# Optimization experiments

Measured on AMD Instinct MI355X. Metric: run time of the kernel, lower is better.

Reference implementation:

```python
import jax, jax.numpy as jnp
import numpy as np

HID, H, KV, D = 2048, 16, 4, 128
B, L = 8, 1024
T = B * L
EPS = 1e-6
NEG = -1e9


def _rms(x, w):
    # RMSNorm over head_dim in fp32
    var = jnp.mean(x.astype(jnp.float32) ** 2, axis=-1, keepdims=True)
    return (x.astype(jnp.float32) * jax.lax.rsqrt(var + EPS)).astype(x.dtype) * w


def _rot_half(x):
    x1, x2 = jnp.split(x, 2, axis=-1)
    return jnp.concatenate([-x2, x1], axis=-1)


def setup_inputs() -> dict:
    key = jax.random.key(0)
    ks = jax.random.split(key, 24)
    inp = {}
    inp['packed_sequence'] = jax.random.normal(ks[0], (T, HID), jnp.float32) * 0.02
    # RoPE tables: positions restart per sample
    pos = jnp.tile(jnp.arange(L, dtype=jnp.float32), B)  # [T]
    inv_freq = 1.0 / (10000.0 ** (jnp.arange(0, D, 2, dtype=jnp.float32) / D))
    ang = pos[:, None] * inv_freq[None, :]  # [T, D/2]
    inp['cos'] = jnp.concatenate([jnp.cos(ang), jnp.cos(ang)], axis=-1)
    inp['sin'] = jnp.concatenate([jnp.sin(ang), jnp.sin(ang)], axis=-1)
    # per-sample causal additive mask [B, L, L]
    causal = jnp.tril(jnp.ones((L, L), bool))
    inp['attn_bias'] = jnp.broadcast_to(jnp.where(causal, 0.0, NEG).astype(jnp.float32), (B, L, L))
    inp['gen_mask'] = jax.random.randint(ks[1], (T,), 0, 2, jnp.int32)
    s = 0.02
    inp['Wq'] = jax.random.normal(ks[2], (H * D, HID), jnp.float32) * s
    inp['bq'] = jnp.zeros((H * D,), jnp.float32)
    inp['Wqg'] = jax.random.normal(ks[3], (H * D, HID), jnp.float32) * s
    inp['bqg'] = jnp.zeros((H * D,), jnp.float32)
    inp['Wk'] = jax.random.normal(ks[4], (KV * D, HID), jnp.float32) * s
    inp['bk'] = jnp.zeros((KV * D,), jnp.float32)
    inp['Wkg'] = jax.random.normal(ks[5], (KV * D, HID), jnp.float32) * s
    inp['bkg'] = jnp.zeros((KV * D,), jnp.float32)
    inp['Wv'] = jax.random.normal(ks[6], (KV * D, HID), jnp.float32) * s
    inp['bv'] = jnp.zeros((KV * D,), jnp.float32)
    inp['Wvg'] = jax.random.normal(ks[7], (KV * D, HID), jnp.float32) * s
    inp['bvg'] = jnp.zeros((KV * D,), jnp.float32)
    inp['Wo'] = jax.random.normal(ks[8], (HID, H * D), jnp.float32) * s
    inp['Wog'] = jax.random.normal(ks[9], (HID, H * D), jnp.float32) * s
    inp['q_norm_w'] = jnp.ones((D,), jnp.float32)
    inp['q_norm_gen_w'] = jnp.ones((D,), jnp.float32)
    inp['k_norm_w'] = jnp.ones((D,), jnp.float32)
    inp['k_norm_gen_w'] = jnp.ones((D,), jnp.float32)
    return inp


def reference(packed_sequence, cos, sin, attn_bias, gen_mask,
              Wq, bq, Wqg, bqg, Wk, bk, Wkg, bkg, Wv, bv, Wvg, bvg,
              Wo, Wog, q_norm_w, q_norm_gen_w, k_norm_w, k_norm_gen_w):
    route = (gen_mask > 0)[:, None]  # [T,1]; und/gen indexes partition tokens -> select
    # dual-path QKV projections (scatter into zero buffers == per-token select)
    q = jnp.where(route, packed_sequence @ Wqg.T + bqg, packed_sequence @ Wq.T + bq)
    k = jnp.where(route, packed_sequence @ Wkg.T + bkg, packed_sequence @ Wk.T + bk)
    v = jnp.where(route, packed_sequence @ Wvg.T + bvg, packed_sequence @ Wv.T + bv)
    q = q.reshape(T, H, D)
    k = k.reshape(T, KV, D)
    v = v.reshape(T, KV, D)
    rh = route[:, :, None]  # [T,1,1]
    # dual-path per-head-dim RMSNorm
    q = jnp.where(rh, _rms(q, q_norm_gen_w), _rms(q, q_norm_w))
    k = jnp.where(rh, _rms(k, k_norm_gen_w), _rms(k, k_norm_w))
    # RoPE (broadcast over heads, unsqueeze_dim=1)
    c, s = cos[:, None, :], sin[:, None, :]
    q = q * c + _rot_half(q) * s
    k = k * c + _rot_half(k) * s
    # GQA: repeat kv heads to H
    k = jnp.repeat(k, H // KV, axis=1)
    v = jnp.repeat(v, H // KV, axis=1)
    # ragged attention, equal sample lens -> batched SDPA with per-sample masks
    qb = q.reshape(B, L, H, D)
    kb = k.reshape(B, L, H, D)
    vb = v.reshape(B, L, H, D)
    scores = jnp.einsum('blhd,bmhd->bhlm', qb, kb) / np.sqrt(D).astype(np.float32)
    scores = scores + attn_bias[:, None, :, :]
    p = jax.nn.softmax(scores, axis=-1)
    o = jnp.einsum('bhlm,bmhd->blhd', p, vb).reshape(T, H * D)
    # dual-path output projection (no bias)
    return jnp.where(route, o @ Wog.T, o @ Wo.T)
```

## Files before the change

kernel.cpp:

```cpp
#include <hip/hip_runtime.h>

#define T_TOK 8192
#define HID   2048
#define NH    16
#define NKV   4
#define HD    128

typedef __attribute__((ext_vector_type(8))) short short8;
typedef __attribute__((ext_vector_type(4))) float f32x4;
typedef __attribute__((ext_vector_type(4))) unsigned short us4;

__device__ __forceinline__ unsigned short f2b(float f) {
  union { float f; unsigned int u; } x; x.f = f;
  unsigned int u = x.u;
  return (unsigned short)((u + 0x7FFFu + ((u >> 16) & 1u)) >> 16);
}
__device__ __forceinline__ float b2f(unsigned short u) {
  union { float f; unsigned int u; } x; x.u = ((unsigned int)u) << 16; return x.f;
}

__device__ __forceinline__ void ld_lds16(const unsigned short* g, unsigned short* l) {
  __builtin_amdgcn_global_load_lds(
      (const __attribute__((address_space(1))) unsigned int*)g,
      (__attribute__((address_space(3))) unsigned int*)l, 16, 0, 0);
}

__global__ __launch_bounds__(1024) void scan_route(const int* __restrict__ gm,
                                                   int* __restrict__ perm,
                                                   int* __restrict__ n0p) {
  __shared__ int cnt[1024];
  int tid = threadIdx.x;
  int base = tid * 8;
  int r[8]; int c0 = 0;
#pragma unroll
  for (int i = 0; i < 8; i++) { r[i] = gm[base + i] > 0 ? 1 : 0; c0 += 1 - r[i]; }
  cnt[tid] = c0;
  __syncthreads();
  for (int off = 1; off < 1024; off <<= 1) {
    int add = (tid >= off) ? cnt[tid - off] : 0;
    __syncthreads();
    cnt[tid] += add;
    __syncthreads();
  }
  int incl = cnt[tid];
  int total0 = cnt[1023];
  int p0 = incl - c0;
  int p1 = total0 + (base - (incl - c0));
#pragma unroll
  for (int i = 0; i < 8; i++) {
    int t = base + i;
    if (r[i] == 0) perm[p0++] = t;
    else           perm[p1++] = t;
  }
  if (tid == 0) n0p[0] = total0;
}

struct ConvArgs {
  const float* src[9];
  unsigned short* dst[9];
  int blk_end[9];
};

__global__ __launch_bounds__(256) void convert_all(ConvArgs a) {
  int blk = blockIdx.x;
  int s = 0;
  while (blk >= a.blk_end[s]) s++;
  int local = blk - (s ? a.blk_end[s - 1] : 0);
  int i = local * 1024 + threadIdx.x * 4;
  float4 v = *(const float4*)(a.src[s] + i);
  us4 o = { f2b(v.x), f2b(v.y), f2b(v.z), f2b(v.w) };
  *(us4*)(a.dst[s] + i) = o;
}

#define BM  128
#define BK  64

__device__ __forceinline__ void gemm_core(
    const unsigned short* __restrict__ Xb,
    const unsigned short* __restrict__ W,
    const float* __restrict__ bias,
    const int* __restrict__ perm,
    int r0, int r1, int col0, int N,
    float* __restrict__ outF, unsigned short* __restrict__ outB,
    unsigned short* As, unsigned short* Bs)
{
  int tid = threadIdx.x;
  int lane = tid & 63, wid = tid >> 6;
  int quad = lane >> 4, l15 = lane & 15;
  int wr = (wid >> 1) * 64, wc = (wid & 1) * 64;
  int lrow = lane >> 3;
  int sc8 = (lane & 7) ^ (lrow & 7);

  const unsigned short* ag[4]; const unsigned short* bg[4];
  unsigned short* al[4]; unsigned short* bl[4];
#pragma unroll
  for (int i = 0; i < 4; i++) {
    int row = wid * 32 + i * 8 + lrow;
    int gr = r0 + row; if (gr > r1 - 1) gr = r1 - 1;
    ag[i] = Xb + (size_t)perm[gr] * HID + sc8 * 8;
    bg[i] = W + (size_t)(col0 + row) * HID + sc8 * 8;
    al[i] = As + (wid * 32 + i * 8) * BK;
    bl[i] = Bs + (wid * 32 + i * 8) * BK;
  }

  f32x4 zero = {0.f, 0.f, 0.f, 0.f};
  f32x4 acc[4][4];
#pragma unroll
  for (int a = 0; a < 4; a++)
#pragma unroll
    for (int b = 0; b < 4; b++) acc[a][b] = zero;

  for (int k0 = 0; k0 < HID; k0 += BK) {
#pragma unroll
    for (int i = 0; i < 4; i++) {
      ld_lds16(ag[i] + k0, al[i]);
      ld_lds16(bg[i] + k0, bl[i]);
    }
    __syncthreads();
#pragma unroll
    for (int kk = 0; kk < 2; kk++) {
      int cswz = ((kk * 4 + quad) ^ (l15 & 7)) * 8;
      short8 af[4], bf[4];
#pragma unroll
      for (int mt = 0; mt < 4; mt++)
        af[mt] = *(const short8*)&As[(wr + mt * 16 + l15) * BK + cswz];
#pragma unroll
      for (int nt = 0; nt < 4; nt++)
        bf[nt] = *(const short8*)&Bs[(wc + nt * 16 + l15) * BK + cswz];
#pragma unroll
      for (int mt = 0; mt < 4; mt++)
#pragma unroll
        for (int nt = 0; nt < 4; nt++)
          acc[mt][nt] = __builtin_amdgcn_mfma_f32_16x16x32_bf16(af[mt], bf[nt], acc[mt][nt], 0, 0, 0);
    }
    __syncthreads();
  }

#pragma unroll
  for (int mt = 0; mt < 4; mt++) {
#pragma unroll
    for (int r = 0; r < 4; r++) {
      int lr = wr + mt * 16 + quad * 4 + r;
      int gr = r0 + lr;
      if (gr >= r1) continue;
      int tok = perm[gr];
#pragma unroll
      for (int nt = 0; nt < 4; nt++) {
        int col = col0 + wc + nt * 16 + l15;
        float v = acc[mt][nt][r];
        if (bias) v += bias[col];
        if (outF) outF[(size_t)tok * N + col] = v;
        else      outB[(size_t)tok * N + col] = f2b(v);
      }
    }
  }
}

__global__ __launch_bounds__(256, 3) void gemm_qkv(
    const unsigned short* __restrict__ xb,
    const unsigned short* wq0, const unsigned short* wq1,
    const float* bq0, const float* bq1,
    const unsigned short* wk0, const unsigned short* wk1,
    const float* bk0, const float* bk1,
    const unsigned short* wv0, const unsigned short* wv1,
    const float* bv0, const float* bv1,
    unsigned short* qraw, unsigned short* kraw, unsigned short* vb,
    const int* __restrict__ perm, const int* __restrict__ n0p)
{
  __shared__ unsigned short As[BM * BK];
  __shared__ unsigned short Bs[BM * BK];
  int set = blockIdx.z;
  int n0 = n0p[0];
  int r0, r1;
  if (set == 0) { r0 = blockIdx.x * BM; if (r0 >= n0) return; r1 = (r0 + BM < n0) ? r0 + BM : n0; }
  else          { r0 = n0 + blockIdx.x * BM; if (r0 >= T_TOK) return; r1 = (r0 + BM < T_TOK) ? r0 + BM : T_TOK; }
  int y = blockIdx.y;
  const unsigned short* w; const float* bias;
  unsigned short* ob; int col0, N;
  if (y < 16)      { w = set ? wq1 : wq0; bias = set ? bq1 : bq0; col0 = y * 128;        N = HID; ob = qraw; }
  else if (y < 20) { w = set ? wk1 : wk0; bias = set ? bk1 : bk0; col0 = (y - 16) * 128; N = 512; ob = kraw; }
  else             { w = set ? wv1 : wv0; bias = set ? bv1 : bv0; col0 = (y - 20) * 128; N = 512; ob = vb; }
  gemm_core(xb, w, bias, perm, r0, r1, col0, N, nullptr, ob, As, Bs);
}

__global__ __launch_bounds__(256, 3) void gemm_out(
    const unsigned short* __restrict__ obuf,
    const unsigned short* wo0, const unsigned short* wo1,
    float* __restrict__ out,
    const int* __restrict__ perm, const int* __restrict__ n0p)
{
  __shared__ unsigned short As[BM * BK];
  __shared__ unsigned short Bs[BM * BK];
  int set = blockIdx.z;
  int n0 = n0p[0];
  int r0, r1;
  if (set == 0) { r0 = blockIdx.x * BM; if (r0 >= n0) return; r1 = (r0 + BM < n0) ? r0 + BM : n0; }
  else          { r0 = n0 + blockIdx.x * BM; if (r0 >= T_TOK) return; r1 = (r0 + BM < T_TOK) ? r0 + BM : T_TOK; }
  gemm_core(obuf, set ? wo1 : wo0, nullptr, perm, r0, r1, blockIdx.y * 128, HID, out, nullptr, As, Bs);
}

__global__ __launch_bounds__(256) void rms_rope_all(
    const unsigned short* __restrict__ qin, unsigned short* __restrict__ qout,
    const unsigned short* __restrict__ kin, unsigned short* __restrict__ kout,
    const float* __restrict__ cosb, const float* __restrict__ sinb,
    const int* __restrict__ gm,
    const float* __restrict__ qwn, const float* __restrict__ qwg,
    const float* __restrict__ kwn, const float* __restrict__ kwg)
{
  int wvid = blockIdx.x * 4 + (threadIdx.x >> 6);
  int lane = threadIdx.x & 63;
  const unsigned short* in; unsigned short* outp;
  const float* wn; const float* wg; int t, h, nh;
  if (wvid < T_TOK * NH) {
    in = qin; outp = qout; wn = qwn; wg = qwg; t = wvid >> 4; h = wvid & 15; nh = NH;
  } else {
    int w2 = wvid - T_TOK * NH;
    in = kin; outp = kout; wn = kwn; wg = kwg; t = w2 >> 2; h = w2 & 3; nh = NKV;
  }
  size_t off = ((size_t)t * nh + h) * HD;
  float x1 = b2f(in[off + lane]), x2 = b2f(in[off + 64 + lane]);
  float ss = x1 * x1 + x2 * x2;
#pragma unroll
  for (int o = 32; o > 0; o >>= 1) ss += __shfl_xor(ss, o, 64);
  float inv = rsqrtf(ss * (1.0f / 128.0f) + 1e-6f);
  const float* w = (gm[t] > 0) ? wg : wn;
  float n1 = x1 * inv * w[lane];
  float n2 = x2 * inv * w[lane + 64];
  float c1 = cosb[t * HD + lane],      s1 = sinb[t * HD + lane];
  float c2 = cosb[t * HD + 64 + lane], s2 = sinb[t * HD + 64 + lane];
  outp[off + lane]      = f2b(n1 * c1 - n2 * s1);
  outp[off + 64 + lane] = f2b(n2 * c2 + n1 * s2);
}

__global__ __launch_bounds__(256) void vtrans(const unsigned short* __restrict__ vb,
                                              unsigned short* __restrict__ vt) {
  __shared__ unsigned short Vs[64][136];
  int kt = blockIdx.x, kvh = blockIdx.y, b = blockIdx.z;
  int t = threadIdx.x;
  int kv0 = kt * 64;
  int key = t >> 2, c0 = t & 3;
#pragma unroll
  for (int i = 0; i < 4; i++) {
    int cc = c0 * 4 + i;
    *(short8*)&Vs[key][cc * 8] =
        *(const short8*)(vb + ((size_t)(b * 1024 + kv0 + key) * NKV + kvh) * HD + cc * 8);
  }
  __syncthreads();
  int d = t >> 1, hh = t & 1;
  unsigned short tmp[32];
#pragma unroll
  for (int k = 0; k < 32; k++) tmp[k] = Vs[hh * 32 + k][d];
  size_t base = ((size_t)(b * NKV + kvh) * HD + d) * 1024 + kv0 + hh * 32;
  *(short8*)(vt + base)      = *(short8*)&tmp[0];
  *(short8*)(vt + base + 8)  = *(short8*)&tmp[8];
  *(short8*)(vt + base + 16) = *(short8*)&tmp[16];
  *(short8*)(vt + base + 24) = *(short8*)&tmp[24];
}

__global__ __launch_bounds__(512, 4) void attn_kernel(
    const unsigned short* __restrict__ qb,
    const unsigned short* __restrict__ kb,
    const unsigned short* __restrict__ vt,
    unsigned short* __restrict__ ob)
{
  __shared__ unsigned short Ks[2][64 * 128];
  __shared__ unsigned short Vt[2][128 * 64];
  __shared__ unsigned short Ps[8 * 16 * 64];
  int pslot = blockIdx.x, kvh = blockIdx.y, b = blockIdx.z;
  int tid = threadIdx.x, lane = tid & 63, wid = tid >> 6;
  int quad = lane >> 4, l15 = lane & 15;
  int h = kvh * 4 + (wid >> 1);
  int g = wid & 1;
  const float sc = 0.088388347648318447f;
  f32x4 zero = {0.f, 0.f, 0.f, 0.f};

  int skey = (wid << 2) + (lane >> 4);
  int kswz = ((lane & 15) ^ (skey & 7)) * 8;
  int sd   = (wid << 3) + (lane >> 3);
  int vswz = ((lane & 7) ^ (sd & 7)) * 8;

  auto stageKV = [&](int buf, int kv0) {
#pragma unroll
    for (int i = 0; i < 2; i++) {
      int key = i * 32 + skey;
      ld_lds16(kb + ((size_t)(b * 1024 + kv0 + key) * NKV + kvh) * HD + kswz,
               &Ks[buf][(size_t)(i * 32 + (wid << 2)) * 128]);
    }
#pragma unroll
    for (int i = 0; i < 2; i++) {
      int d = i * 64 + sd;
      ld_lds16(vt + ((size_t)(b * NKV + kvh) * HD + d) * 1024 + kv0 + vswz,
               &Vt[buf][(size_t)(i * 64 + (wid << 3)) * 64]);
    }
  };

  for (int half = 0; half < 2; half++) {
    int a = half ? (31 - pslot) : pslot;
    int q0 = a * 32;
    int qrow = q0 + g * 16 + l15;
    size_t qoff = ((size_t)(b * 1024 + qrow) * NH + h) * HD;
    short8 qfr[4];
#pragma unroll
    for (int kk = 0; kk < 4; kk++)
      qfr[kk] = *(const short8*)(qb + qoff + kk * 32 + quad * 8);

    f32x4 oacc[8];
#pragma unroll
    for (int i = 0; i < 8; i++) oacc[i] = zero;
    float lpart[4] = {0.f, 0.f, 0.f, 0.f};

    int ktiles = a / 2 + 1;
    stageKV(0, 0);
    int cur = 0;

    for (int kt = 0; kt < ktiles; kt++) {
      int kv0 = kt * 64;
      bool hasnext = (kt + 1 < ktiles);
      if (hasnext) {
        stageKV(cur ^ 1, kv0 + 64);
        asm volatile("s_waitcnt vmcnt(4)" ::: "memory");
      } else {
        asm volatile("s_waitcnt vmcnt(0)" ::: "memory");
      }
      __builtin_amdgcn_s_barrier();
      __builtin_amdgcn_sched_barrier(0);
      const unsigned short* ksb = Ks[cur];
      const unsigned short* vvb = Vt[cur];
      bool lastt = (kt == ktiles - 1);

      f32x4 s[4];
      __builtin_amdgcn_s_setprio(1);
#pragma unroll
      for (int g4 = 0; g4 < 4; g4++) {
        f32x4 acc = zero;
#pragma unroll
        for (int kk = 0; kk < 4; kk++) {
          short8 bfr = *(const short8*)&ksb[(g4 * 16 + l15) * 128 + ((kk * 4 + quad) ^ (l15 & 7)) * 8];
          acc = __builtin_amdgcn_mfma_f32_16x16x32_bf16(qfr[kk], bfr, acc, 0, 0, 0);
        }
        s[g4] = acc;
      }
      __builtin_amdgcn_s_setprio(0);

      int rowb = q0 + g * 16 + quad * 4;
#pragma unroll
      for (int g4 = 0; g4 < 4; g4++) {
        int col = kv0 + g4 * 16 + l15;
        int k8 = g4 * 2 + (l15 >> 3);
#pragma unroll
        for (int r = 0; r < 4; r++) {
          float p = __expf(s[g4][r] * sc);
          if (lastt && col > rowb + r) p = 0.f;
          lpart[r] += p;
          int row = quad * 4 + r;
          Ps[wid * 1024 + row * 64 + ((k8 ^ (row & 7)) * 8 + (l15 & 7))] = f2b(p);
        }
      }

      __builtin_amdgcn_s_setprio(1);
#pragma unroll
      for (int kk = 0; kk < 2; kk++) {
        short8 pa = *(const short8*)&Ps[wid * 1024 + l15 * 64 + ((kk * 4 + quad) ^ (l15 & 7)) * 8];
#pragma unroll
        for (int dg = 0; dg < 8; dg++) {
          short8 vf = *(const short8*)&vvb[(dg * 16 + l15) * 64 + ((kk * 4 + quad) ^ (l15 & 7)) * 8];
          oacc[dg] = __builtin_amdgcn_mfma_f32_16x16x32_bf16(pa, vf, oacc[dg], 0, 0, 0);
        }
      }
      __builtin_amdgcn_s_setprio(0);

      __builtin_amdgcn_s_barrier();
      __builtin_amdgcn_sched_barrier(0);
      cur ^= 1;
    }

#pragma unroll
    for (int r = 0; r < 4; r++) {
      float v = lpart[r];
#pragma unroll
      for (int o = 8; o > 0; o >>= 1) v += __shfl_xor(v, o, 64);
      lpart[r] = 1.0f / v;
    }
#pragma unroll
    for (int dg = 0; dg < 8; dg++)
#pragma unroll
      for (int r = 0; r < 4; r++) {
        int row = q0 + g * 16 + quad * 4 + r;
        ob[((size_t)(b * 1024 + row) * NH + h) * HD + dg * 16 + l15] =
            f2b(oacc[dg][r] * lpart[r]);
      }
  }
}

extern "C" void kernel_launch(void* const* d_in, const int* in_sizes, int n_in,
                              void* d_out, int out_size, void* d_ws, size_t ws_size,
                              hipStream_t stream) {
  const float* x    = (const float*)d_in[0];
  const float* cosb = (const float*)d_in[1];
  const float* sinb = (const float*)d_in[2];
  const int*   gm   = (const int*)d_in[4];
  const float* Wq   = (const float*)d_in[5];
  const float* bq   = (const float*)d_in[6];
  const float* Wqg  = (const float*)d_in[7];
  const float* bqg  = (const float*)d_in[8];
  const float* Wk   = (const float*)d_in[9];
  const float* bk   = (const float*)d_in[10];
  const float* Wkg  = (const float*)d_in[11];
  const float* bkg  = (const float*)d_in[12];
  const float* Wv   = (const float*)d_in[13];
  const float* bv   = (const float*)d_in[14];
  const float* Wvg  = (const float*)d_in[15];
  const float* bvg  = (const float*)d_in[16];
  const float* Wo   = (const float*)d_in[17];
  const float* Wog  = (const float*)d_in[18];
  const float* qnw  = (const float*)d_in[19];
  const float* qngw = (const float*)d_in[20];
  const float* knw  = (const float*)d_in[21];
  const float* kngw = (const float*)d_in[22];
  float* out = (float*)d_out;

  char* wsb = (char*)d_ws;
  size_t off = 0;
  auto alloc = [&](size_t bytes) -> char* {
    char* p = wsb + off;
    off += (bytes + 255) & ~(size_t)255;
    return p;
  };
  int* perm = (int*)alloc((size_t)T_TOK * 4);
  int* n0p  = (int*)alloc(4);
  unsigned short* xb  = (unsigned short*)alloc((size_t)T_TOK * HID * 2);
  unsigned short* wq0 = (unsigned short*)alloc((size_t)HID * HID * 2);
  unsigned short* wq1 = (unsigned short*)alloc((size_t)HID * HID * 2);
  unsigned short* wk0 = (unsigned short*)alloc((size_t)512 * HID * 2);
  unsigned short* wk1 = (unsigned short*)alloc((size_t)512 * HID * 2);
  unsigned short* wv0 = (unsigned short*)alloc((size_t)512 * HID * 2);
  unsigned short* wv1 = (unsigned short*)alloc((size_t)512 * HID * 2);
  unsigned short* wo0 = (unsigned short*)alloc((size_t)HID * HID * 2);
  unsigned short* wo1 = (unsigned short*)alloc((size_t)HID * HID * 2);
  unsigned short* qraw = (unsigned short*)alloc((size_t)T_TOK * HID * 2);
  unsigned short* kraw = (unsigned short*)alloc((size_t)T_TOK * 512 * 2);
  unsigned short* vbuf = (unsigned short*)alloc((size_t)T_TOK * 512 * 2);
  unsigned short* vtb  = (unsigned short*)alloc((size_t)T_TOK * 512 * 2);
  unsigned short* qbuf = (unsigned short*)alloc((size_t)T_TOK * HID * 2);
  unsigned short* kbuf = (unsigned short*)alloc((size_t)T_TOK * 512 * 2);
  unsigned short* obuf = qraw;

  scan_route<<<dim3(1), dim3(1024), 0, stream>>>(gm, perm, n0p);

  ConvArgs ca;
  const float* srcs[9] = {x, Wq, Wqg, Wk, Wkg, Wv, Wvg, Wo, Wog};
  unsigned short* dsts[9] = {xb, wq0, wq1, wk0, wk1, wv0, wv1, wo0, wo1};
  int ns[9] = {T_TOK * HID, HID * HID, HID * HID, 512 * HID, 512 * HID,
               512 * HID, 512 * HID, HID * HID, HID * HID};
  int cum = 0;
  for (int i = 0; i < 9; i++) {
    ca.src[i] = srcs[i]; ca.dst[i] = dsts[i];
    cum += ns[i] / 1024; ca.blk_end[i] = cum;
  }
  convert_all<<<dim3(cum), dim3(256), 0, stream>>>(ca);

  gemm_qkv<<<dim3(64, 24, 2), dim3(256), 0, stream>>>(
      xb, wq0, wq1, bq, bqg, wk0, wk1, bk, bkg, wv0, wv1, bv, bvg,
      qraw, kraw, vbuf, perm, n0p);

  rms_rope_all<<<dim3(T_TOK * (NH + NKV) / 4), dim3(256), 0, stream>>>(
      qraw, qbuf, kraw, kbuf, cosb, sinb, gm, qnw, qngw, knw, kngw);
  vtrans<<<dim3(16, 4, 8), dim3(256), 0, stream>>>(vbuf, vtb);

  attn_kernel<<<dim3(16, 4, 8), dim3(512), 0, stream>>>(qbuf, kbuf, vtb, obuf);

  gemm_out<<<dim3(64, 16, 2), dim3(256), 0, stream>>>(obuf, wo0, wo1, out, perm, n0p);
}
```

Measured before the change: 567.2 us.

## Rewrite projection GEMMs as 256x256 double-buffered 8-wave pipelined kernel

Replaces the 128x128 single-buffered GEMM core with a 256x256 tile computed by 8 waves, using double-buffered LDS and staggered async global->LDS loads interleaved with MFMA phases, plus s_setprio around the math. The goal is to hide global load latency behind compute and raise data reuse per tile, cutting the per-iteration barrier stalls of the old kernel. It uses 128KB of LDS per block and larger accumulators, which lowers occupancy. Bigger tiles also waste more work on the partial tiles at the route-split boundary.

```diff
diff --git a/kernel.cpp b/kernel.cpp
--- a/kernel.cpp
+++ b/kernel.cpp
@@ -72,10 +72,11 @@
   *(us4*)(a.dst[s] + i) = o;
 }
 
-#define BM  128
-#define BK  64
-
-__device__ __forceinline__ void gemm_core(
+#define BM2 256
+#define BK2 64
+#define NT2 (HID / BK2)
+
+__device__ __forceinline__ void gemm8(
     const unsigned short* __restrict__ Xb,
     const unsigned short* __restrict__ W,
     const float* __restrict__ bias,
@@ -87,67 +88,108 @@
   int tid = threadIdx.x;
   int lane = tid & 63, wid = tid >> 6;
   int quad = lane >> 4, l15 = lane & 15;
-  int wr = (wid >> 1) * 64, wc = (wid & 1) * 64;
-  int lrow = lane >> 3;
-  int sc8 = (lane & 7) ^ (lrow & 7);
-
-  const unsigned short* ag[4]; const unsigned short* bg[4];
-  unsigned short* al[4]; unsigned short* bl[4];
-#pragma unroll
-  for (int i = 0; i < 4; i++) {
-    int row = wid * 32 + i * 8 + lrow;
-    int gr = r0 + row; if (gr > r1 - 1) gr = r1 - 1;
-    ag[i] = Xb + (size_t)perm[gr] * HID + sc8 * 8;
-    bg[i] = W + (size_t)(col0 + row) * HID + sc8 * 8;
-    al[i] = As + (wid * 32 + i * 8) * BK;
-    bl[i] = Bs + (wid * 32 + i * 8) * BK;
-  }
+  int wr2 = (wid >> 2) * 128;
+  int wc2 = (wid & 3) * 64;
+
+  const unsigned short* aptr[2][2];
+  const unsigned short* bptr[2][2];
+  int ldso[2][2];
+#pragma unroll
+  for (int h = 0; h < 2; h++)
+#pragma unroll
+    for (int r = 0; r < 2; r++) {
+      int row = h * 128 + r * 64 + wid * 8 + (lane >> 3);
+      int cs = ((lane & 7) ^ (row & 7)) * 8;
+      int gr = r0 + row; if (gr > r1 - 1) gr = r1 - 1;
+      aptr[h][r] = Xb + (size_t)perm[gr] * HID + cs;
+      bptr[h][r] = W + (size_t)(col0 + row) * HID + cs;
+      ldso[h][r] = (h * 128 + r * 64 + wid * 8) * BK2;
+    }
 
   f32x4 zero = {0.f, 0.f, 0.f, 0.f};
-  f32x4 acc[4][4];
-#pragma unroll
-  for (int a = 0; a < 4; a++)
-#pragma unroll
-    for (int b = 0; b < 4; b++) acc[a][b] = zero;
-
-  for (int k0 = 0; k0 < HID; k0 += BK) {
-#pragma unroll
-    for (int i = 0; i < 4; i++) {
-      ld_lds16(ag[i] + k0, al[i]);
-      ld_lds16(bg[i] + k0, bl[i]);
-    }
-    __syncthreads();
-#pragma unroll
-    for (int kk = 0; kk < 2; kk++) {
-      int cswz = ((kk * 4 + quad) ^ (l15 & 7)) * 8;
-      short8 af[4], bf[4];
-#pragma unroll
-      for (int mt = 0; mt < 4; mt++)
-        af[mt] = *(const short8*)&As[(wr + mt * 16 + l15) * BK + cswz];
-#pragma unroll
-      for (int nt = 0; nt < 4; nt++)
-        bf[nt] = *(const short8*)&Bs[(wc + nt * 16 + l15) * BK + cswz];
-#pragma unroll
-      for (int mt = 0; mt < 4; mt++)
-#pragma unroll
-        for (int nt = 0; nt < 4; nt++)
-          acc[mt][nt] = __builtin_amdgcn_mfma_f32_16x16x32_bf16(af[mt], bf[nt], acc[mt][nt], 0, 0, 0);
-    }
-    __syncthreads();
-  }
-
-#pragma unroll
-  for (int mt = 0; mt < 4; mt++) {
-#pragma unroll
-    for (int r = 0; r < 4; r++) {
-      int lr = wr + mt * 16 + quad * 4 + r;
+  f32x4 acc[8][4];
+#pragma unroll
+  for (int m = 0; m < 8; m++)
+#pragma unroll
+    for (int n = 0; n < 4; n++) acc[m][n] = zero;
+
+  auto stgA = [&](int buf, int t, int h) {
+#pragma unroll
+    for (int r = 0; r < 2; r++)
+      ld_lds16(aptr[h][r] + t * BK2, As + buf * (BM2 * BK2) + ldso[h][r]);
+  };
+  auto stgB = [&](int buf, int t, int h) {
+#pragma unroll
+    for (int r = 0; r < 2; r++)
+      ld_lds16(bptr[h][r] + t * BK2, Bs + buf * (BM2 * BK2) + ldso[h][r]);
+  };
+
+  stgA(0, 0, 0); stgA(0, 0, 1); stgB(0, 0, 0); stgB(0, 0, 1);
+  stgB(1, 1, 0); stgB(1, 1, 1);
+  asm volatile("s_waitcnt vmcnt(4)" ::: "memory");
+  __builtin_amdgcn_s_barrier();
+
+  for (int t = 0; t < NT2; t++) {
+    int cur = t & 1;
+    const unsigned short* Ab = As + cur * (BM2 * BK2);
+    const unsigned short* Bb = Bs + cur * (BM2 * BK2);
+    short8 bf[4][2];
+#pragma unroll
+    for (int p = 0; p < 4; p++) {
+      if (p == 0) {
+#pragma unroll
+        for (int n = 0; n < 4; n++)
+#pragma unroll
+          for (int kk = 0; kk < 2; kk++)
+            bf[n][kk] = *(const short8*)&Bb[(wc2 + n * 16 + l15) * BK2 +
+                                            (((kk * 4 + quad) ^ (l15 & 7)) * 8)];
+      }
+      short8 af[2][2];
+#pragma unroll
+      for (int mi = 0; mi < 2; mi++)
+#pragma unroll
+        for (int kk = 0; kk < 2; kk++)
+          af[mi][kk] = *(const short8*)&Ab[(wr2 + (p * 2 + mi) * 16 + l15) * BK2 +
+                                           (((kk * 4 + quad) ^ (l15 & 7)) * 8)];
+      if (p == 0)      { if (t + 1 < NT2) stgA(cur ^ 1, t + 1, 0); }
+      else if (p == 1) { if (t + 1 < NT2) stgA(cur ^ 1, t + 1, 1); }
+      else if (p == 2) { if (t + 2 < NT2) stgB(cur, t + 2, 0); }
+      else             { if (t + 2 < NT2) stgB(cur, t + 2, 1); }
+
+      __builtin_amdgcn_s_barrier();
+      asm volatile("s_waitcnt lgkmcnt(0)" ::: "memory");
+      __builtin_amdgcn_s_setprio(1);
+#pragma unroll
+      for (int mi = 0; mi < 2; mi++)
+#pragma unroll
+        for (int n = 0; n < 4; n++)
+#pragma unroll
+          for (int kk = 0; kk < 2; kk++)
+            acc[p * 2 + mi][n] = __builtin_amdgcn_mfma_f32_16x16x32_bf16(
+                af[mi][kk], bf[n][kk], acc[p * 2 + mi][n], 0, 0, 0);
+      __builtin_amdgcn_s_setprio(0);
+      if (p < 3) {
+        __builtin_amdgcn_s_barrier();
+      } else {
+        if (t + 2 < NT2) asm volatile("s_waitcnt vmcnt(4)" ::: "memory");
+        else             asm volatile("s_waitcnt vmcnt(0)" ::: "memory");
+        __builtin_amdgcn_s_barrier();
+      }
+    }
+  }
+
+#pragma unroll
+  for (int m = 0; m < 8; m++) {
+#pragma unroll
+    for (int rr = 0; rr < 4; rr++) {
+      int lr = wr2 + m * 16 + quad * 4 + rr;
       int gr = r0 + lr;
       if (gr >= r1) continue;
       int tok = perm[gr];
 #pragma unroll
-      for (int nt = 0; nt < 4; nt++) {
-        int col = col0 + wc + nt * 16 + l15;
-        float v = acc[mt][nt][r];
+      for (int n = 0; n < 4; n++) {
+        int col = col0 + wc2 + n * 16 + l15;
+        float v = acc[m][n][rr];
         if (bias) v += bias[col];
         if (outF) outF[(size_t)tok * N + col] = v;
         else      outB[(size_t)tok * N + col] = f2b(v);
@@ -156,7 +198,7 @@
   }
 }
 
-__global__ __launch_bounds__(256, 3) void gemm_qkv(
+__global__ __launch_bounds__(512, 2) void gemm_qkv(
     const unsigned short* __restrict__ xb,
     const unsigned short* wq0, const unsigned short* wq1,
     const float* bq0, const float* bq1,
@@ -167,36 +209,36 @@
     unsigned short* qraw, unsigned short* kraw, unsigned short* vb,
     const int* __restrict__ perm, const int* __restrict__ n0p)
 {
-  __shared__ unsigned short As[BM * BK];
-  __shared__ unsigned short Bs[BM * BK];
+  __shared__ unsigned short As[2 * BM2 * BK2];
+  __shared__ unsigned short Bs[2 * BM2 * BK2];
   int set = blockIdx.z;
   int n0 = n0p[0];
   int r0, r1;
-  if (set == 0) { r0 = blockIdx.x * BM; if (r0 >= n0) return; r1 = (r0 + BM < n0) ? r0 + BM : n0; }
-  else          { r0 = n0 + blockIdx.x * BM; if (r0 >= T_TOK) return; r1 = (r0 + BM < T_TOK) ? r0 + BM : T_TOK; }
+  if (set == 0) { r0 = blockIdx.x * BM2; if (r0 >= n0) return; r1 = (r0 + BM2 < n0) ? r0 + BM2 : n0; }
+  else          { r0 = n0 + blockIdx.x * BM2; if (r0 >= T_TOK) return; r1 = (r0 + BM2 < T_TOK) ? r0 + BM2 : T_TOK; }
   int y = blockIdx.y;
   const unsigned short* w; const float* bias;
   unsigned short* ob; int col0, N;
-  if (y < 16)      { w = set ? wq1 : wq0; bias = set ? bq1 : bq0; col0 = y * 128;        N = HID; ob = qraw; }
-  else if (y < 20) { w = set ? wk1 : wk0; bias = set ? bk1 : bk0; col0 = (y - 16) * 128; N = 512; ob = kraw; }
-  else             { w = set ? wv1 : wv0; bias = set ? bv1 : bv0; col0 = (y - 20) * 128; N = 512; ob = vb; }
-  gemm_core(xb, w, bias, perm, r0, r1, col0, N, nullptr, ob, As, Bs);
-}
-
-__global__ __launch_bounds__(256, 3) void gemm_out(
+  if (y < 8)       { w = set ? wq1 : wq0; bias = set ? bq1 : bq0; col0 = y * 256;        N = HID; ob = qraw; }
+  else if (y < 10) { w = set ? wk1 : wk0; bias = set ? bk1 : bk0; col0 = (y - 8) * 256;  N = 512; ob = kraw; }
+  else             { w = set ? wv1 : wv0; bias = set ? bv1 : bv0; col0 = (y - 10) * 256; N = 512; ob = vb; }
+  gemm8(xb, w, bias, perm, r0, r1, col0, N, nullptr, ob, As, Bs);
+}
+
+__global__ __launch_bounds__(512, 2) void gemm_out(
     const unsigned short* __restrict__ obuf,
     const unsigned short* wo0, const unsigned short* wo1,
     float* __restrict__ out,
     const int* __restrict__ perm, const int* __restrict__ n0p)
 {
-  __shared__ unsigned short As[BM * BK];
-  __shared__ unsigned short Bs[BM * BK];
+  __shared__ unsigned short As[2 * BM2 * BK2];
+  __shared__ unsigned short Bs[2 * BM2 * BK2];
   int set = blockIdx.z;
   int n0 = n0p[0];
   int r0, r1;
-  if (set == 0) { r0 = blockIdx.x * BM; if (r0 >= n0) return; r1 = (r0 + BM < n0) ? r0 + BM : n0; }
-  else          { r0 = n0 + blockIdx.x * BM; if (r0 >= T_TOK) return; r1 = (r0 + BM < T_TOK) ? r0 + BM : T_TOK; }
-  gemm_core(obuf, set ? wo1 : wo0, nullptr, perm, r0, r1, blockIdx.y * 128, HID, out, nullptr, As, Bs);
+  if (set == 0) { r0 = blockIdx.x * BM2; if (r0 >= n0) return; r1 = (r0 + BM2 < n0) ? r0 + BM2 : n0; }
+  else          { r0 = n0 + blockIdx.x * BM2; if (r0 >= T_TOK) return; r1 = (r0 + BM2 < T_TOK) ? r0 + BM2 : T_TOK; }
+  gemm8(obuf, set ? wo1 : wo0, nullptr, perm, r0, r1, blockIdx.y * 256, HID, out, nullptr, As, Bs);
 }
 
 __global__ __launch_bounds__(256) void rms_rope_all(
@@ -459,7 +501,7 @@
   }
   convert_all<<<dim3(cum), dim3(256), 0, stream>>>(ca);
 
-  gemm_qkv<<<dim3(64, 24, 2), dim3(256), 0, stream>>>(
+  gemm_qkv<<<dim3(32, 12, 2), dim3(512), 0, stream>>>(
       xb, wq0, wq1, bq, bqg, wk0, wk1, bk, bkg, wv0, wv1, bv, bvg,
       qraw, kraw, vbuf, perm, n0p);
 
@@ -469,5 +511,5 @@
 
   attn_kernel<<<dim3(16, 4, 8), dim3(512), 0, stream>>>(qbuf, kbuf, vtb, obuf);
 
-  gemm_out<<<dim3(64, 16, 2), dim3(256), 0, stream>>>(obuf, wo0, wo1, out, perm, n0p);
-}
+  gemm_out<<<dim3(32, 8, 2), dim3(512), 0, stream>>>(obuf, wo0, wo1, out, perm, n0p);
+}
```

New measurement: 696.0 us. 1.23x slower.
